# Kernel tuning notes

Hardware: AMD Instinct MI355X
Metric: run time of the kernel (lower is better)

The kernel has to match this reference:

```python
import jax, jax.numpy as jnp
import numpy as np

N, D, H, L, GHD, OUT = 512, 128, 4, 4, 32, 128  # nodes, input_dim, heads, layers, graph_hidden_dim, output_dim


def _xavier(key, shape):
    fan_in, fan_out = shape[0], shape[1]
    limit = float(np.sqrt(6.0 / (fan_in + fan_out)))
    return jax.random.uniform(key, shape, jnp.float32, -limit, limit)


def setup_inputs() -> dict:
    key = jax.random.key(0)
    ks = jax.random.split(key, 16)
    node_feat = jax.random.normal(ks[0], (N, D), jnp.float32)
    edge_feat = jax.random.normal(ks[1], (N, N, D), jnp.float32)
    adj = jax.random.uniform(ks[2], (H, N, N), jnp.float32)
    # per-(head,layer) edge weights: all [D, GHD]
    W_edge = _xavier(ks[3], (D, GHD))[None, None] * jnp.ones((H, L, 1, 1), jnp.float32)
    W_edge = jax.random.uniform(ks[3], (H, L, D, GHD), jnp.float32, -0.1, 0.1)
    # per-layer node weights (input dim grows by GHD each layer): [H, D + l*GHD, GHD]
    Wn0 = _xavier(ks[4], (D + 0 * GHD, GHD))[None] * jnp.ones((H, 1, 1), jnp.float32)
    Wn0 = jax.random.uniform(ks[4], (H, D + 0 * GHD, GHD), jnp.float32, -0.1, 0.1)
    Wn1 = jax.random.uniform(ks[5], (H, D + 1 * GHD, GHD), jnp.float32, -0.1, 0.1)
    Wn2 = jax.random.uniform(ks[6], (H, D + 2 * GHD, GHD), jnp.float32, -0.1, 0.1)
    Wn3 = jax.random.uniform(ks[7], (H, D + 3 * GHD, GHD), jnp.float32, -0.1, 0.1)
    # final linear: in = hidden_dim * head_num = L*GHD*H = 512, out = OUT
    W_lin = _xavier(ks[8], (L * GHD * H, OUT))
    b_lin = jnp.zeros((OUT,), jnp.float32)
    return {"node_feat": node_feat, "edge_feat": edge_feat, "adj": adj,
            "W_edge": W_edge, "Wn0": Wn0, "Wn1": Wn1, "Wn2": Wn2, "Wn3": Wn3,
            "W_lin": W_lin, "b_lin": b_lin}


def reference(node_feat, edge_feat, adj, W_edge, Wn0, Wn1, Wn2, Wn3, W_lin, b_lin):
    # mean over second node axis; einsum('ijk,kp->ijp') then mean(dim=1) == mean then matmul
    edge_mean = jnp.mean(edge_feat, axis=1)  # [N, D]
    Wn = [Wn0, Wn1, Wn2, Wn3]
    head_feats = []
    for h in range(H):
        A = adj[h]                         # [N, N]
        deg = jnp.sum(A, axis=1)           # [N]
        denom = (deg + (deg == 0).astype(deg.dtype))[:, None]  # zero-degree -> divide by 1
        outputs = node_feat
        cache = [node_feat]
        outs = []
        for l in range(L):
            e_out = edge_mean @ W_edge[h, l]            # [N, GHD]
            n_out = A @ (outputs @ Wn[l][h])            # chain_matmul(A, X, W)
            g = jax.nn.relu((e_out + n_out) / denom)    # [N, GHD]
            cache.append(g)
            outputs = jnp.concatenate(cache, axis=-1)
            outs.append(g)                              # dropout is eval-mode identity
        head_feats.append(jnp.concatenate(outs, axis=-1) + node_feat)  # [N, D]
    all_heads = jnp.concatenate(head_feats, axis=-1)    # [N, H*D]
    return all_heads @ W_lin + b_lin                    # [N, OUT]
```

## Files before the change

### kernel.cpp

```cpp
#include <hip/hip_runtime.h>
#include <cstddef>

#define NN 512
#define DD 128
#define HH 4
#define LL 4
#define GHD 32
#define OUTD 128

static constexpr size_t OFF_EP  = 0;
static constexpr size_t OFF_ANF = OFF_EP  + (size_t)4 * NN * DD;
static constexpr size_t OFF_DEN = OFF_ANF + (size_t)HH * NN * DD;
static constexpr size_t OFF_EO  = OFF_DEN + (size_t)HH * NN;
static constexpr size_t OFF_G   = OFF_EO  + (size_t)HH * LL * NN * GHD;
static constexpr size_t OFF_AG  = OFF_G   + (size_t)HH * LL * NN * GHD;

__global__ __launch_bounds__(256) void prep_kernel(
    const float* __restrict__ node_feat,
    const float* __restrict__ edge_feat,
    const float* __restrict__ adj,
    float* __restrict__ ws)
{
    const int t = threadIdx.x;
    const int b = blockIdx.x;
    __shared__ __align__(16) float smem[4 * NN + 256];

    if (b >= 512) {
        const int bb = b - 512;
        const int r  = bb >> 2;
        const int jq = bb & 3;
        const int q  = t & 31;
        const int g  = t >> 5;
        const float4* ef = reinterpret_cast<const float4*>(edge_feat)
                         + ((size_t)r * NN + (size_t)jq * 128) * (DD / 4);
        float4 acc; acc.x = acc.y = acc.z = acc.w = 0.f;
        #pragma unroll
        for (int k = 0; k < 16; ++k) {
            float4 v = ef[(size_t)(g + 8 * k) * (DD / 4) + q];
            acc.x += v.x; acc.y += v.y; acc.z += v.z; acc.w += v.w;
        }
        float4* red = reinterpret_cast<float4*>(smem);
        red[t] = acc;
        __syncthreads();
        for (int s = 128; s >= 32; s >>= 1) {
            if (t < s) {
                float4 o = red[t + s], m = red[t];
                m.x += o.x; m.y += o.y; m.z += o.z; m.w += o.w;
                red[t] = m;
            }
            __syncthreads();
        }
        if (t < 32)
            reinterpret_cast<float4*>(ws + OFF_EP + ((size_t)jq * NN + r) * DD)[t] = red[t];
    } else {
        const int h  = b >> 7;
        const int r0 = (b & 127) * 4;
        const float* A = adj + (size_t)h * NN * NN;
        float* Arow = smem;
        float* dred = smem + 4 * NN;

        for (int idx = t; idx < 4 * NN; idx += 256)
            Arow[idx] = A[(size_t)r0 * NN + idx];
        __syncthreads();

        {
            const int rr = t >> 6, lane = t & 63;
            float s = 0.f;
            #pragma unroll 8
            for (int j = lane; j < NN; j += 64) s += Arow[rr * NN + j];
            dred[t] = s;
            __syncthreads();
            if (t < 4) {
                float d = 0.f;
                for (int j = 0; j < 64; ++j) d += dred[t * 64 + j];
                ws[OFF_DEN + (size_t)h * NN + r0 + t] = d + (d == 0.f ? 1.f : 0.f);
            }
        }

        const int c  = t & 127;
        const int rb = t >> 7;
        float a0 = 0.f, a1 = 0.f;
        #pragma unroll 4
        for (int j = 0; j < NN; ++j) {
            float nf = node_feat[(size_t)j * DD + c];
            a0 += Arow[(rb + 0) * NN + j] * nf;
            a1 += Arow[(rb + 2) * NN + j] * nf;
        }
        float* anf = ws + OFF_ANF + ((size_t)h * NN + r0) * DD;
        anf[(rb + 0) * DD + c] = a0;
        anf[(rb + 2) * DD + c] = a1;
    }
}

__global__ __launch_bounds__(256) void eout_kernel(
    const float* __restrict__ W_edge,
    float* __restrict__ ws)
{
    const int b  = blockIdx.x;
    const int rg = b & 31;
    const int hl = b >> 5;
    const int r0 = rg * 16;
    const int t  = threadIdx.x;
    __shared__ float em[16 * DD];

    const float* P = ws + OFF_EP;
    for (int idx = t; idx < 16 * DD; idx += 256) {
        int r = r0 + (idx >> 7), k = idx & 127;
        size_t o = (size_t)r * DD + k;
        em[idx] = (P[o] + P[(size_t)NN * DD + o]
                 + P[2 * (size_t)NN * DD + o] + P[3 * (size_t)NN * DD + o])
                * (1.0f / (float)NN);
    }
    __syncthreads();

    const int c  = t & 31;
    const int rr = t >> 5;
    const float* We = W_edge + (size_t)hl * DD * GHD;
    float s0 = 0.f, s1 = 0.f;
    #pragma unroll 4
    for (int k = 0; k < DD; ++k) {
        float w = We[(size_t)k * GHD + c];
        s0 += em[rr * DD + k] * w;
        s1 += em[(rr + 8) * DD + k] * w;
    }
    float* eo = ws + OFF_EO + ((size_t)hl * NN + r0) * GHD;
    eo[(size_t)rr * GHD + c]       = s0;
    eo[(size_t)(rr + 8) * GHD + c] = s1;
}

template <int L>
__global__ __launch_bounds__(256) void layer_kernel(
    const float* __restrict__ adj,
    const float* __restrict__ Wn,
    float* __restrict__ ws)
{
    constexpr int KIN = DD + GHD * L;
    const int b   = blockIdx.x;
    const int h   = b >> 8;
    const int r0  = (b & 255) * 2;
    const int t   = threadIdx.x;
    const int rr  = t >> 7;
    const int sub = (t >> 5) & 3;
    const int c   = t & 31;
    const int r   = r0 + rr;

    const float* anf = ws + OFF_ANF;
    const float* den = ws + OFF_DEN;
    const float* eo  = ws + OFF_EO;
    float* G  = ws + OFF_G;
    float* AG = ws + OFF_AG;

    __shared__ float smem[256 + 64 + 256];
    float* agp = smem;
    float* agl = smem + 256;
    float* pp  = smem + 320;

    if (L > 0) {
        const float4* A4 = reinterpret_cast<const float4*>(
            adj + ((size_t)h * NN + r) * NN);
        const float* gp = G + (((size_t)h * LL + (L - 1)) * NN) * GHD;
        float s = 0.f;
        #pragma unroll 4
        for (int j4 = sub * 32; j4 < sub * 32 + 32; ++j4) {
            float4 a = A4[j4];
            const float* gj = gp + (size_t)j4 * 4 * GHD + c;
            s += a.x * gj[0] + a.y * gj[GHD] + a.z * gj[2 * GHD] + a.w * gj[3 * GHD];
        }
        agp[t] = s;
    }
    __syncthreads();
    if (L > 0 && sub == 0) {
        float ag = agp[rr * 128 + c] + agp[rr * 128 + 32 + c]
                 + agp[rr * 128 + 64 + c] + agp[rr * 128 + 96 + c];
        AG[(((size_t)h * 3 + (L - 1)) * NN + r) * GHD + c] = ag;
        agl[rr * GHD + c] = ag;
    }
    __syncthreads();

    float p = 0.f;
    {
        const float* Wnl = Wn + (size_t)h * KIN * GHD;
        const float* ar  = anf + ((size_t)h * NN + r) * DD;
        #pragma unroll 8
        for (int k = sub * 32; k < sub * 32 + 32; ++k)
            p += ar[k] * Wnl[(size_t)k * GHD + c];
        if (sub < L) {
            const float* agk = (sub == L - 1)
                ? (agl + rr * GHD)
                : (AG + (((size_t)h * 3 + sub) * NN + r) * GHD);
            const float* w = Wnl + (size_t)(DD + sub * GHD) * GHD + c;
            #pragma unroll 8
            for (int m = 0; m < GHD; ++m)
                p += agk[m] * w[(size_t)m * GHD];
        }
    }
    pp[t] = p;
    __syncthreads();
    if (sub == 0) {
        float tot = pp[rr * 128 + c] + pp[rr * 128 + 32 + c]
                  + pp[rr * 128 + 64 + c] + pp[rr * 128 + 96 + c]
                  + eo[(((size_t)h * LL + L) * NN + r) * GHD + c];
        float dn = den[(size_t)h * NN + r];
        float gv = tot / dn;
        gv = gv > 0.f ? gv : 0.f;
        G[(((size_t)h * LL + L) * NN + r) * GHD + c] = gv;
    }
}

__global__ __launch_bounds__(256) void final_kernel(
    const float* __restrict__ node_feat,
    const float* __restrict__ W_lin,
    const float* __restrict__ b_lin,
    const float* __restrict__ ws,
    float* __restrict__ out)
{
    const int b  = blockIdx.x;
    const int n  = b >> 1;
    const int oh = b & 1;
    const int t  = threadIdx.x;
    const int ol = t & 63;
    const int ks = t >> 6;
    const int o  = oh * 64 + ol;
    const float* G = ws + OFF_G;
    __shared__ float red[256];

    float p = 0.f;
    #pragma unroll
    for (int l = 0; l < LL; ++l) {
        const float* gr  = G + (((size_t)ks * LL + l) * NN + n) * GHD;
        const float* nfr = node_feat + (size_t)n * DD + l * GHD;
        const float* w   = W_lin + (size_t)(ks * DD + l * GHD) * OUTD + o;
        #pragma unroll 8
        for (int cc = 0; cc < GHD; ++cc)
            p += (gr[cc] + nfr[cc]) * w[(size_t)cc * OUTD];
    }
    red[t] = p;
    __syncthreads();
    if (ks == 0)
        out[(size_t)n * OUTD + o] =
            red[ol] + red[64 + ol] + red[128 + ol] + red[192 + ol] + b_lin[o];
}

extern "C" void kernel_launch(void* const* d_in, const int* in_sizes, int n_in,
                              void* d_out, int out_size, void* d_ws, size_t ws_size,
                              hipStream_t stream)
{
    const float* node_feat = (const float*)d_in[0];
    const float* edge_feat = (const float*)d_in[1];
    const float* adj       = (const float*)d_in[2];
    const float* W_edge    = (const float*)d_in[3];
    const float* Wn0       = (const float*)d_in[4];
    const float* Wn1       = (const float*)d_in[5];
    const float* Wn2       = (const float*)d_in[6];
    const float* Wn3       = (const float*)d_in[7];
    const float* W_lin     = (const float*)d_in[8];
    const float* b_lin     = (const float*)d_in[9];
    float* out = (float*)d_out;
    float* ws  = (float*)d_ws;

    hipLaunchKernelGGL(prep_kernel, dim3(512 + 2048), dim3(256), 0, stream,
                       node_feat, edge_feat, adj, ws);
    hipLaunchKernelGGL(eout_kernel, dim3(512), dim3(256), 0, stream, W_edge, ws);
    hipLaunchKernelGGL(layer_kernel<0>, dim3(1024), dim3(256), 0, stream, adj, Wn0, ws);
    hipLaunchKernelGGL(layer_kernel<1>, dim3(1024), dim3(256), 0, stream, adj, Wn1, ws);
    hipLaunchKernelGGL(layer_kernel<2>, dim3(1024), dim3(256), 0, stream, adj, Wn2, ws);
    hipLaunchKernelGGL(layer_kernel<3>, dim3(1024), dim3(256), 0, stream, adj, Wn3, ws);
    hipLaunchKernelGGL(final_kernel, dim3(1024), dim3(256), 0, stream,
                       node_feat, W_lin, b_lin, ws, out);
}
```

Baseline: 330.8 us.

## Fuse all stages into one cooperative persistent kernel with grid syncs

```diff
diff --git a/kernel.cpp b/kernel.cpp
--- a/kernel.cpp
+++ b/kernel.cpp
@@ -1,5 +1,8 @@
 #include <hip/hip_runtime.h>
+#include <hip/hip_cooperative_groups.h>
 #include <cstddef>
+
+namespace cg = cooperative_groups;
 
 #define NN 512
 #define DD 128
@@ -14,6 +17,249 @@
 static constexpr size_t OFF_EO  = OFF_DEN + (size_t)HH * NN;
 static constexpr size_t OFF_G   = OFF_EO  + (size_t)HH * LL * NN * GHD;
 static constexpr size_t OFF_AG  = OFF_G   + (size_t)HH * LL * NN * GHD;
+
+__device__ __forceinline__ void f4acc(float4& a, const float4& v) {
+    a.x += v.x; a.y += v.y; a.z += v.z; a.w += v.w;
+}
+
+__global__ __launch_bounds__(256, 2) void fused_kernel(
+    const float* __restrict__ node_feat,
+    const float* __restrict__ edge_feat,
+    const float* __restrict__ adj,
+    const float* __restrict__ W_edge,
+    const float* __restrict__ Wn0,
+    const float* __restrict__ Wn1,
+    const float* __restrict__ Wn2,
+    const float* __restrict__ Wn3,
+    const float* __restrict__ W_lin,
+    const float* __restrict__ b_lin,
+    float* __restrict__ ws,
+    float* __restrict__ out)
+{
+    cg::grid_group grid = cg::this_grid();
+    const int t = threadIdx.x;
+    const int b = blockIdx.x;
+
+    __shared__ __align__(16) float smem[8192];
+
+    float* EM  = ws + OFF_EP;
+    float* ANF = ws + OFF_ANF;
+    float* DEN = ws + OFF_DEN;
+    float* EO  = ws + OFF_EO;
+    float* G   = ws + OFF_G;
+    float* AG  = ws + OFF_AG;
+
+    {
+        const float4* efb = reinterpret_cast<const float4*>(edge_feat)
+                          + (size_t)b * (NN * DD / 4);
+        float4 a0{0,0,0,0}, a1{0,0,0,0}, a2{0,0,0,0}, a3{0,0,0,0};
+        #pragma unroll
+        for (int m = 0; m < 16; ++m) {
+            float4 v0 = efb[(4*m + 0) * 256 + t];
+            float4 v1 = efb[(4*m + 1) * 256 + t];
+            float4 v2 = efb[(4*m + 2) * 256 + t];
+            float4 v3 = efb[(4*m + 3) * 256 + t];
+            f4acc(a0, v0); f4acc(a1, v1); f4acc(a2, v2); f4acc(a3, v3);
+        }
+        f4acc(a0, a1); f4acc(a2, a3); f4acc(a0, a2);
+        float4* red = reinterpret_cast<float4*>(smem);
+        red[t] = a0;
+        __syncthreads();
+        if (t < 128) f4acc(red[t], red[t + 128]);
+        __syncthreads();
+        if (t < 64)  f4acc(red[t], red[t + 64]);
+        __syncthreads();
+        if (t < 32) {
+            float4 m = red[t];
+            f4acc(m, red[t + 32]);
+            const float inv = 1.0f / (float)NN;
+            m.x *= inv; m.y *= inv; m.z *= inv; m.w *= inv;
+            reinterpret_cast<float4*>(EM + (size_t)b * DD)[t] = m;
+        }
+        __syncthreads();
+    }
+
+    if (b < 128) {
+        const int h  = b >> 5;
+        const int r0 = (b & 31) * 16;
+        float4* As4 = reinterpret_cast<float4*>(smem);
+        const float4* Ad4 = reinterpret_cast<const float4*>(
+            adj + ((size_t)h * NN + r0) * NN);
+        #pragma unroll
+        for (int u = 0; u < 8; ++u) As4[t + u * 256] = Ad4[t + u * 256];
+        __syncthreads();
+        const float* Arow = smem;
+
+        {
+            const int rl = t >> 4, ln = t & 15;
+            float s = 0.f;
+            #pragma unroll 8
+            for (int j = ln; j < NN; j += 16) s += Arow[rl * NN + j];
+            #pragma unroll
+            for (int m = 8; m >= 1; m >>= 1) s += __shfl_xor(s, m);
+            if (ln == 0)
+                DEN[(size_t)h * NN + r0 + rl] = s + (s == 0.f ? 1.f : 0.f);
+        }
+
+        const int c = t & 127, rg = t >> 7;
+        float c0=0,c1=0,c2=0,c3=0,c4=0,c5=0,c6=0,c7=0;
+        #pragma unroll 4
+        for (int j = 0; j < NN; ++j) {
+            float nf = node_feat[(size_t)j * DD + c];
+            c0 += Arow[(rg +  0) * NN + j] * nf;
+            c1 += Arow[(rg +  2) * NN + j] * nf;
+            c2 += Arow[(rg +  4) * NN + j] * nf;
+            c3 += Arow[(rg +  6) * NN + j] * nf;
+            c4 += Arow[(rg +  8) * NN + j] * nf;
+            c5 += Arow[(rg + 10) * NN + j] * nf;
+            c6 += Arow[(rg + 12) * NN + j] * nf;
+            c7 += Arow[(rg + 14) * NN + j] * nf;
+        }
+        float* ab = ANF + ((size_t)h * NN + r0) * DD + c;
+        ab[(rg +  0) * DD] = c0; ab[(rg +  2) * DD] = c1;
+        ab[(rg +  4) * DD] = c2; ab[(rg +  6) * DD] = c3;
+        ab[(rg +  8) * DD] = c4; ab[(rg + 10) * DD] = c5;
+        ab[(rg + 12) * DD] = c6; ab[(rg + 14) * DD] = c7;
+    }
+
+    grid.sync();
+
+    const int h  = b >> 7;
+    const int r0 = (b & 127) * 4;
+    const int c  = t & 31;
+    const int ks = (t >> 5) & 1;
+    const int rr = t >> 6;
+    const int r  = r0 + rr;
+
+    float* emS   = smem;
+    float* anfS  = smem + 512;
+    float* aglS  = smem + 1024;
+    float* pred  = smem + 1152;
+    float* ArowS = smem + 1408;
+
+    emS[t]        = EM[((size_t)r0 + (t >> 7)) * DD + (t & 127)];
+    emS[t + 256]  = EM[((size_t)r0 + 2 + (t >> 7)) * DD + (t & 127)];
+    anfS[t]       = ANF[((size_t)h * NN + r0 + (t >> 7)) * DD + (t & 127)];
+    anfS[t + 256] = ANF[((size_t)h * NN + r0 + 2 + (t >> 7)) * DD + (t & 127)];
+    __syncthreads();
+
+    float eo0 = 0.f;
+    #pragma unroll
+    for (int l = 0; l < 4; ++l) {
+        const float* We = W_edge + ((size_t)(h * LL + l) * DD) * GHD;
+        float p = 0.f;
+        #pragma unroll 8
+        for (int k = ks * 64; k < ks * 64 + 64; ++k)
+            p += emS[rr * DD + k] * We[(size_t)k * GHD + c];
+        pred[t] = p;
+        __syncthreads();
+        if (ks == 0) {
+            float v = pred[t] + pred[t + 32];
+            if (l == 0) eo0 = v;
+            else EO[((size_t)(h * LL + l) * NN + r) * GHD + c] = v;
+        }
+        __syncthreads();
+    }
+    {
+        const float* W0 = Wn0 + (size_t)h * DD * GHD;
+        float p = 0.f;
+        #pragma unroll 8
+        for (int k = ks * 64; k < ks * 64 + 64; ++k)
+            p += anfS[rr * DD + k] * W0[(size_t)k * GHD + c];
+        pred[t] = p;
+        __syncthreads();
+        if (ks == 0) {
+            float v = pred[t] + pred[t + 32] + eo0;
+            v /= DEN[(size_t)h * NN + r];
+            v = v > 0.f ? v : 0.f;
+            G[((size_t)(h * LL + 0) * NN + r) * GHD + c] = v;
+        }
+    }
+
+    #pragma unroll
+    for (int l = 1; l < 4; ++l) {
+        grid.sync();
+        if (l == 1) {
+            float4* As4 = reinterpret_cast<float4*>(ArowS);
+            const float4* Ad4 = reinterpret_cast<const float4*>(
+                adj + ((size_t)h * NN + r0) * NN);
+            As4[t]       = Ad4[t];
+            As4[t + 256] = Ad4[t + 256];
+            __syncthreads();
+        }
+        {
+            const float* gp = G + ((size_t)(h * LL + l - 1) * NN) * GHD;
+            const float4* Ar4 = reinterpret_cast<const float4*>(ArowS);
+            float s = 0.f;
+            #pragma unroll 4
+            for (int j4 = ks * 64; j4 < ks * 64 + 64; ++j4) {
+                float4 a = Ar4[rr * 128 + j4];
+                const float* gj = gp + (size_t)j4 * 4 * GHD + c;
+                s += a.x * gj[0] + a.y * gj[GHD]
+                   + a.z * gj[2 * GHD] + a.w * gj[3 * GHD];
+            }
+            pred[t] = s;
+            __syncthreads();
+            if (ks == 0) {
+                float ag = pred[t] + pred[t + 32];
+                AG[((size_t)(h * 3 + l - 1) * NN + r) * GHD + c] = ag;
+                aglS[rr * GHD + c] = ag;
+            }
+            __syncthreads();
+        }
+        const float* Wnb = (l == 1) ? Wn1 : (l == 2) ? Wn2 : Wn3;
+        const float* Wnl = Wnb + (size_t)h * (DD + GHD * l) * GHD;
+        float p = 0.f;
+        #pragma unroll 8
+        for (int k = ks * 64; k < ks * 64 + 64; ++k)
+            p += anfS[rr * DD + k] * Wnl[(size_t)k * GHD + c];
+        #pragma unroll
+        for (int kk = 0; kk < l; ++kk) {
+            if ((kk & 1) == ks) {
+                const float* agv = (kk == l - 1)
+                    ? (aglS + rr * GHD)
+                    : (AG + ((size_t)(h * 3 + kk) * NN + r) * GHD);
+                const float* w = Wnl + ((size_t)(DD + kk * GHD)) * GHD + c;
+                #pragma unroll 8
+                for (int m = 0; m < GHD; ++m)
+                    p += agv[m] * w[(size_t)m * GHD];
+            }
+        }
+        pred[t] = p;
+        __syncthreads();
+        if (ks == 0) {
+            float v = pred[t] + pred[t + 32]
+                    + EO[((size_t)(h * LL + l) * NN + r) * GHD + c];
+            v /= DEN[(size_t)h * NN + r];
+            v = v > 0.f ? v : 0.f;
+            G[((size_t)(h * LL + l) * NN + r) * GHD + c] = v;
+        }
+    }
+
+    grid.sync();
+
+    {
+        const int n  = b;
+        const int o  = t & 127;
+        const int hs = t >> 7;
+        float p = 0.f;
+        for (int hh = hs; hh < HH; hh += 2) {
+            #pragma unroll
+            for (int l2 = 0; l2 < LL; ++l2) {
+                const float* gr  = G + ((size_t)(hh * LL + l2) * NN + n) * GHD;
+                const float* nfr = node_feat + (size_t)n * DD + l2 * GHD;
+                const float* w   = W_lin + (size_t)(hh * DD + l2 * GHD) * OUTD + o;
+                #pragma unroll 8
+                for (int cc = 0; cc < GHD; ++cc)
+                    p += (gr[cc] + nfr[cc]) * w[(size_t)cc * OUTD];
+            }
+        }
+        smem[t] = p;
+        __syncthreads();
+        if (hs == 0)
+            out[(size_t)n * OUTD + o] = smem[o] + smem[o + 128] + b_lin[o];
+    }
+}
 
 __global__ __launch_bounds__(256) void prep_kernel(
     const float* __restrict__ node_feat,
@@ -33,21 +279,17 @@
         const int g  = t >> 5;
         const float4* ef = reinterpret_cast<const float4*>(edge_feat)
                          + ((size_t)r * NN + (size_t)jq * 128) * (DD / 4);
-        float4 acc; acc.x = acc.y = acc.z = acc.w = 0.f;
+        float4 acc{0,0,0,0};
         #pragma unroll
         for (int k = 0; k < 16; ++k) {
             float4 v = ef[(size_t)(g + 8 * k) * (DD / 4) + q];
-            acc.x += v.x; acc.y += v.y; acc.z += v.z; acc.w += v.w;
+            f4acc(acc, v);
         }
         float4* red = reinterpret_cast<float4*>(smem);
         red[t] = acc;
         __syncthreads();
         for (int s = 128; s >= 32; s >>= 1) {
-            if (t < s) {
-                float4 o = red[t + s], m = red[t];
-                m.x += o.x; m.y += o.y; m.z += o.z; m.w += o.w;
-                red[t] = m;
-            }
+            if (t < s) f4acc(red[t], red[t + s]);
             __syncthreads();
         }
         if (t < 32)
@@ -62,7 +304,6 @@
         for (int idx = t; idx < 4 * NN; idx += 256)
             Arow[idx] = A[(size_t)r0 * NN + idx];
         __syncthreads();
-
         {
             const int rr = t >> 6, lane = t & 63;
             float s = 0.f;
@@ -76,7 +317,6 @@
                 ws[OFF_DEN + (size_t)h * NN + r0 + t] = d + (d == 0.f ? 1.f : 0.f);
             }
         }
-
         const int c  = t & 127;
         const int rb = t >> 7;
         float a0 = 0.f, a1 = 0.f;
@@ -258,13 +498,24 @@
     float* out = (float*)d_out;
     float* ws  = (float*)d_ws;
 
-    hipLaunchKernelGGL(prep_kernel, dim3(512 + 2048), dim3(256), 0, stream,
-                       node_feat, edge_feat, adj, ws);
-    hipLaunchKernelGGL(eout_kernel, dim3(512), dim3(256), 0, stream, W_edge, ws);
-    hipLaunchKernelGGL(layer_kernel<0>, dim3(1024), dim3(256), 0, stream, adj, Wn0, ws);
-    hipLaunchKernelGGL(layer_kernel<1>, dim3(1024), dim3(256), 0, stream, adj, Wn1, ws);
-    hipLaunchKernelGGL(layer_kernel<2>, dim3(1024), dim3(256), 0, stream, adj, Wn2, ws);
-    hipLaunchKernelGGL(layer_kernel<3>, dim3(1024), dim3(256), 0, stream, adj, Wn3, ws);
-    hipLaunchKernelGGL(final_kernel, dim3(1024), dim3(256), 0, stream,
-                       node_feat, W_lin, b_lin, ws, out);
-}
+    void* args[] = {
+        (void*)&node_feat, (void*)&edge_feat, (void*)&adj, (void*)&W_edge,
+        (void*)&Wn0, (void*)&Wn1, (void*)&Wn2, (void*)&Wn3,
+        (void*)&W_lin, (void*)&b_lin, (void*)&ws, (void*)&out
+    };
+    hipError_t rc = hipLaunchCooperativeKernel(
+        reinterpret_cast<void*>(fused_kernel),
+        dim3(512), dim3(256), args, 0, stream);
+
+    if (rc != hipSuccess) {
+        hipLaunchKernelGGL(prep_kernel, dim3(512 + 2048), dim3(256), 0, stream,
+                           node_feat, edge_feat, adj, ws);
+        hipLaunchKernelGGL(eout_kernel, dim3(512), dim3(256), 0, stream, W_edge, ws);
+        hipLaunchKernelGGL(layer_kernel<0>, dim3(1024), dim3(256), 0, stream, adj, Wn0, ws);
+        hipLaunchKernelGGL(layer_kernel<1>, dim3(1024), dim3(256), 0, stream, adj, Wn1, ws);
+        hipLaunchKernelGGL(layer_kernel<2>, dim3(1024), dim3(256), 0, stream, adj, Wn2, ws);
+        hipLaunchKernelGGL(layer_kernel<3>, dim3(1024), dim3(256), 0, stream, adj, Wn3, ws);
+        hipLaunchKernelGGL(final_kernel, dim3(1024), dim3(256), 0, stream,
+                           node_feat, W_lin, b_lin, ws, out);
+    }
+}
```

Measured after the change: 617.3 us. 1.87x slower.

## Fuse prep, edge-output and layer-0 into one kernel; fuse layer-3 with final linear

Applied to the files above, without the earlier changes.

```diff
diff --git a/kernel.cpp b/kernel.cpp
--- a/kernel.cpp
+++ b/kernel.cpp
@@ -8,124 +8,148 @@
 #define GHD 32
 #define OUTD 128
 
-static constexpr size_t OFF_EP  = 0;
-static constexpr size_t OFF_ANF = OFF_EP  + (size_t)4 * NN * DD;
+static constexpr size_t OFF_ANF = 0;
 static constexpr size_t OFF_DEN = OFF_ANF + (size_t)HH * NN * DD;
 static constexpr size_t OFF_EO  = OFF_DEN + (size_t)HH * NN;
 static constexpr size_t OFF_G   = OFF_EO  + (size_t)HH * LL * NN * GHD;
 static constexpr size_t OFF_AG  = OFF_G   + (size_t)HH * LL * NN * GHD;
 
-__global__ __launch_bounds__(256) void prep_kernel(
+__device__ __forceinline__ void f4acc(float4& a, const float4& v) {
+    a.x += v.x; a.y += v.y; a.z += v.z; a.w += v.w;
+}
+
+__global__ __launch_bounds__(256, 2) void k1_prep(
     const float* __restrict__ node_feat,
     const float* __restrict__ edge_feat,
     const float* __restrict__ adj,
+    const float* __restrict__ W_edge,
+    const float* __restrict__ Wn0,
     float* __restrict__ ws)
 {
+    const int r = blockIdx.x;
     const int t = threadIdx.x;
-    const int b = blockIdx.x;
-    __shared__ __align__(16) float smem[4 * NN + 256];
-
-    if (b >= 512) {
-        const int bb = b - 512;
-        const int r  = bb >> 2;
-        const int jq = bb & 3;
-        const int q  = t & 31;
-        const int g  = t >> 5;
-        const float4* ef = reinterpret_cast<const float4*>(edge_feat)
-                         + ((size_t)r * NN + (size_t)jq * 128) * (DD / 4);
-        float4 acc; acc.x = acc.y = acc.z = acc.w = 0.f;
-        #pragma unroll
-        for (int k = 0; k < 16; ++k) {
-            float4 v = ef[(size_t)(g + 8 * k) * (DD / 4) + q];
-            acc.x += v.x; acc.y += v.y; acc.z += v.z; acc.w += v.w;
-        }
-        float4* red = reinterpret_cast<float4*>(smem);
-        red[t] = acc;
-        __syncthreads();
-        for (int s = 128; s >= 32; s >>= 1) {
-            if (t < s) {
-                float4 o = red[t + s], m = red[t];
-                m.x += o.x; m.y += o.y; m.z += o.z; m.w += o.w;
-                red[t] = m;
+
+    __shared__ __align__(16) float4 red4[256];
+    __shared__ float ArowS[4 * NN];
+    __shared__ float emS[DD];
+    __shared__ float anfS[4 * DD];
+    __shared__ float eo0S[4 * GHD];
+    __shared__ float denS[4];
+    __shared__ float pred[256];
+
+    float* ANF = ws + OFF_ANF;
+    float* DEN = ws + OFF_DEN;
+    float* EO  = ws + OFF_EO;
+    float* G   = ws + OFF_G;
+
+    {
+        const float4* efb = reinterpret_cast<const float4*>(edge_feat)
+                          + (size_t)r * (NN * DD / 4);
+        const int m0 = r & 63;
+        float4 acc[8];
+        #pragma unroll
+        for (int u = 0; u < 8; ++u) acc[u] = float4{0, 0, 0, 0};
+        #pragma unroll
+        for (int batch = 0; batch < 4; ++batch) {
+            float4 v[16];
+            #pragma unroll
+            for (int u = 0; u < 16; ++u) {
+                int mm = (m0 + batch * 16 + u) & 63;
+                v[u] = efb[(size_t)mm * 256 + t];
             }
-            __syncthreads();
-        }
-        if (t < 32)
-            reinterpret_cast<float4*>(ws + OFF_EP + ((size_t)jq * NN + r) * DD)[t] = red[t];
-    } else {
-        const int h  = b >> 7;
-        const int r0 = (b & 127) * 4;
-        const float* A = adj + (size_t)h * NN * NN;
-        float* Arow = smem;
-        float* dred = smem + 4 * NN;
-
-        for (int idx = t; idx < 4 * NN; idx += 256)
-            Arow[idx] = A[(size_t)r0 * NN + idx];
-        __syncthreads();
-
-        {
-            const int rr = t >> 6, lane = t & 63;
-            float s = 0.f;
-            #pragma unroll 8
-            for (int j = lane; j < NN; j += 64) s += Arow[rr * NN + j];
-            dred[t] = s;
-            __syncthreads();
-            if (t < 4) {
-                float d = 0.f;
-                for (int j = 0; j < 64; ++j) d += dred[t * 64 + j];
-                ws[OFF_DEN + (size_t)h * NN + r0 + t] = d + (d == 0.f ? 1.f : 0.f);
-            }
-        }
-
-        const int c  = t & 127;
-        const int rb = t >> 7;
+            #pragma unroll
+            for (int u = 0; u < 16; ++u) f4acc(acc[u & 7], v[u]);
+        }
+        #pragma unroll
+        for (int u = 1; u < 8; ++u) f4acc(acc[0], acc[u]);
+        red4[t] = acc[0];
+        __syncthreads();
+        if (t < 128) f4acc(red4[t], red4[t + 128]);
+        __syncthreads();
+        if (t < 64)  f4acc(red4[t], red4[t + 64]);
+        __syncthreads();
+        if (t < 32) {
+            float4 m = red4[t];
+            f4acc(m, red4[t + 32]);
+            const float inv = 1.0f / (float)NN;
+            m.x *= inv; m.y *= inv; m.z *= inv; m.w *= inv;
+            reinterpret_cast<float4*>(emS)[t] = m;
+        }
+    }
+
+    {
+        float4* As4 = reinterpret_cast<float4*>(ArowS);
+        const float4* adj4 = reinterpret_cast<const float4*>(adj);
+        #pragma unroll
+        for (int u = 0; u < 2; ++u) {
+            int idx = u * 256 + t;
+            int h = idx >> 7, j4 = idx & 127;
+            As4[idx] = adj4[(size_t)h * (NN * NN / 4) + (size_t)r * (NN / 4) + j4];
+        }
+    }
+    __syncthreads();
+
+    {
+        const int w = t >> 6, ln = t & 63;
+        float s = 0.f;
+        #pragma unroll
+        for (int j = 0; j < 8; ++j) s += ArowS[w * NN + ln + j * 64];
+        #pragma unroll
+        for (int m = 32; m >= 1; m >>= 1) s += __shfl_xor(s, m);
+        if (ln == 0) {
+            float d = s + (s == 0.f ? 1.f : 0.f);
+            denS[w] = d;
+            DEN[(size_t)w * NN + r] = d;
+        }
+    }
+
+    {
+        const int c = t & 127, hp = t >> 7;
         float a0 = 0.f, a1 = 0.f;
-        #pragma unroll 4
+        #pragma unroll 8
         for (int j = 0; j < NN; ++j) {
             float nf = node_feat[(size_t)j * DD + c];
-            a0 += Arow[(rb + 0) * NN + j] * nf;
-            a1 += Arow[(rb + 2) * NN + j] * nf;
-        }
-        float* anf = ws + OFF_ANF + ((size_t)h * NN + r0) * DD;
-        anf[(rb + 0) * DD + c] = a0;
-        anf[(rb + 2) * DD + c] = a1;
-    }
-}
-
-__global__ __launch_bounds__(256) void eout_kernel(
-    const float* __restrict__ W_edge,
-    float* __restrict__ ws)
-{
-    const int b  = blockIdx.x;
-    const int rg = b & 31;
-    const int hl = b >> 5;
-    const int r0 = rg * 16;
-    const int t  = threadIdx.x;
-    __shared__ float em[16 * DD];
-
-    const float* P = ws + OFF_EP;
-    for (int idx = t; idx < 16 * DD; idx += 256) {
-        int r = r0 + (idx >> 7), k = idx & 127;
-        size_t o = (size_t)r * DD + k;
-        em[idx] = (P[o] + P[(size_t)NN * DD + o]
-                 + P[2 * (size_t)NN * DD + o] + P[3 * (size_t)NN * DD + o])
-                * (1.0f / (float)NN);
-    }
-    __syncthreads();
-
-    const int c  = t & 31;
-    const int rr = t >> 5;
-    const float* We = W_edge + (size_t)hl * DD * GHD;
-    float s0 = 0.f, s1 = 0.f;
-    #pragma unroll 4
-    for (int k = 0; k < DD; ++k) {
-        float w = We[(size_t)k * GHD + c];
-        s0 += em[rr * DD + k] * w;
-        s1 += em[(rr + 8) * DD + k] * w;
-    }
-    float* eo = ws + OFF_EO + ((size_t)hl * NN + r0) * GHD;
-    eo[(size_t)rr * GHD + c]       = s0;
-    eo[(size_t)(rr + 8) * GHD + c] = s1;
+            a0 += ArowS[hp * NN + j] * nf;
+            a1 += ArowS[(hp + 2) * NN + j] * nf;
+        }
+        anfS[hp * DD + c]       = a0;
+        anfS[(hp + 2) * DD + c] = a1;
+        ANF[((size_t)hp * NN + r) * DD + c]       = a0;
+        ANF[((size_t)(hp + 2) * NN + r) * DD + c] = a1;
+    }
+
+    {
+        const int c = t & 31, g = t >> 5;
+        float e0 = 0.f, e1 = 0.f;
+        #pragma unroll 8
+        for (int k = 0; k < DD; ++k) {
+            float e = emS[k];
+            e0 += e * W_edge[((size_t)g * DD + k) * GHD + c];
+            e1 += e * W_edge[((size_t)(g + 8) * DD + k) * GHD + c];
+        }
+        EO[((size_t)g * NN + r) * GHD + c]       = e0;
+        EO[((size_t)(g + 8) * NN + r) * GHD + c] = e1;
+        if ((g & 3) == 0)       eo0S[(g >> 2) * GHD + c]       = e0;
+        if (((g + 8) & 3) == 0) eo0S[((g + 8) >> 2) * GHD + c] = e1;
+    }
+    __syncthreads();
+
+    {
+        const int h = t >> 6, kh = (t >> 5) & 1, c = t & 31;
+        const float* W0 = Wn0 + (size_t)h * DD * GHD;
+        float p = 0.f;
+        #pragma unroll 8
+        for (int k = kh * 64; k < kh * 64 + 64; ++k)
+            p += anfS[h * DD + k] * W0[(size_t)k * GHD + c];
+        pred[t] = p;
+        __syncthreads();
+        if (kh == 0) {
+            float v = p + pred[t + 32] + eo0S[h * GHD + c];
+            v /= denS[h];
+            v = v > 0.f ? v : 0.f;
+            G[((size_t)(h * LL + 0) * NN + r) * GHD + c] = v;
+        }
+    }
 }
 
 template <int L>
@@ -155,12 +179,12 @@
     float* agl = smem + 256;
     float* pp  = smem + 320;
 
-    if (L > 0) {
+    {
         const float4* A4 = reinterpret_cast<const float4*>(
             adj + ((size_t)h * NN + r) * NN);
         const float* gp = G + (((size_t)h * LL + (L - 1)) * NN) * GHD;
         float s = 0.f;
-        #pragma unroll 4
+        #pragma unroll 8
         for (int j4 = sub * 32; j4 < sub * 32 + 32; ++j4) {
             float4 a = A4[j4];
             const float* gj = gp + (size_t)j4 * 4 * GHD + c;
@@ -169,7 +193,7 @@
         agp[t] = s;
     }
     __syncthreads();
-    if (L > 0 && sub == 0) {
+    if (sub == 0) {
         float ag = agp[rr * 128 + c] + agp[rr * 128 + 32 + c]
                  + agp[rr * 128 + 64 + c] + agp[rr * 128 + 96 + c];
         AG[(((size_t)h * 3 + (L - 1)) * NN + r) * GHD + c] = ag;
@@ -185,13 +209,13 @@
         for (int k = sub * 32; k < sub * 32 + 32; ++k)
             p += ar[k] * Wnl[(size_t)k * GHD + c];
         if (sub < L) {
-            const float* agk = (sub == L - 1)
+            const float* agv = (sub == L - 1)
                 ? (agl + rr * GHD)
                 : (AG + (((size_t)h * 3 + sub) * NN + r) * GHD);
             const float* w = Wnl + (size_t)(DD + sub * GHD) * GHD + c;
             #pragma unroll 8
             for (int m = 0; m < GHD; ++m)
-                p += agk[m] * w[(size_t)m * GHD];
+                p += agv[m] * w[(size_t)m * GHD];
         }
     }
     pp[t] = p;
@@ -207,38 +231,131 @@
     }
 }
 
-__global__ __launch_bounds__(256) void final_kernel(
+__global__ __launch_bounds__(256) void k4_last(
     const float* __restrict__ node_feat,
+    const float* __restrict__ adj,
+    const float* __restrict__ Wn3,
     const float* __restrict__ W_lin,
     const float* __restrict__ b_lin,
     const float* __restrict__ ws,
     float* __restrict__ out)
 {
-    const int b  = blockIdx.x;
-    const int n  = b >> 1;
-    const int oh = b & 1;
-    const int t  = threadIdx.x;
-    const int ol = t & 63;
-    const int ks = t >> 6;
-    const int o  = oh * 64 + ol;
-    const float* G = ws + OFF_G;
-    __shared__ float red[256];
-
-    float p = 0.f;
-    #pragma unroll
-    for (int l = 0; l < LL; ++l) {
-        const float* gr  = G + (((size_t)ks * LL + l) * NN + n) * GHD;
-        const float* nfr = node_feat + (size_t)n * DD + l * GHD;
-        const float* w   = W_lin + (size_t)(ks * DD + l * GHD) * OUTD + o;
-        #pragma unroll 8
-        for (int cc = 0; cc < GHD; ++cc)
-            p += (gr[cc] + nfr[cc]) * w[(size_t)cc * OUTD];
-    }
-    red[t] = p;
-    __syncthreads();
-    if (ks == 0)
-        out[(size_t)n * OUTD + o] =
-            red[ol] + red[64 + ol] + red[128 + ol] + red[192 + ol] + b_lin[o];
+    const int r = blockIdx.x;
+    const int t = threadIdx.x;
+
+    __shared__ float ArowS[4 * NN];
+    __shared__ float anfS[4 * DD];
+    __shared__ float nfS[DD];
+    __shared__ float ag2S[4 * GHD];
+    __shared__ float g3S[4 * GHD];
+    __shared__ float denS[4];
+    __shared__ float Xs[4 * DD];
+    __shared__ float pred[256];
+
+    const float* ANF = ws + OFF_ANF;
+    const float* DEN = ws + OFF_DEN;
+    const float* EO  = ws + OFF_EO;
+    const float* G   = ws + OFF_G;
+    const float* AG  = ws + OFF_AG;
+
+    {
+        float4* As4 = reinterpret_cast<float4*>(ArowS);
+        const float4* adj4 = reinterpret_cast<const float4*>(adj);
+        #pragma unroll
+        for (int u = 0; u < 2; ++u) {
+            int idx = u * 256 + t;
+            int h = idx >> 7, j4 = idx & 127;
+            As4[idx] = adj4[(size_t)h * (NN * NN / 4) + (size_t)r * (NN / 4) + j4];
+        }
+        #pragma unroll
+        for (int u = 0; u < 2; ++u) {
+            int idx = u * 256 + t;
+            int h = idx >> 7, k = idx & 127;
+            anfS[idx] = ANF[((size_t)h * NN + r) * DD + k];
+        }
+        if (t < DD) nfS[t] = node_feat[(size_t)r * DD + t];
+        if (t < 4)  denS[t] = DEN[(size_t)t * NN + r];
+    }
+    __syncthreads();
+
+    {
+        const int h = t >> 6, jh = (t >> 5) & 1, c = t & 31;
+        const float* g2 = G + ((size_t)(h * LL + 2) * NN) * GHD;
+        float s = 0.f;
+        #pragma unroll 8
+        for (int j = jh * 256; j < jh * 256 + 256; ++j)
+            s += ArowS[h * NN + j] * g2[(size_t)j * GHD + c];
+        pred[t] = s;
+        __syncthreads();
+        if (jh == 0) ag2S[h * GHD + c] = s + pred[t + 32];
+        __syncthreads();
+    }
+
+    {
+        const int h = t >> 6, kh = (t >> 5) & 1, c = t & 31;
+        const float* W3 = Wn3 + (size_t)h * 224 * GHD;
+        float p = 0.f;
+        #pragma unroll 8
+        for (int k = kh * 64; k < kh * 64 + 64; ++k)
+            p += anfS[h * DD + k] * W3[(size_t)k * GHD + c];
+        if (kh == 0) {
+            const float* ag0 = AG + ((size_t)(h * 3 + 0) * NN + r) * GHD;
+            const float* w   = W3 + (size_t)DD * GHD + c;
+            #pragma unroll 8
+            for (int m = 0; m < GHD; ++m)
+                p += ag0[m] * w[(size_t)m * GHD];
+            const float* w2 = W3 + (size_t)(DD + 2 * GHD) * GHD + c;
+            #pragma unroll 8
+            for (int m = 0; m < GHD; ++m)
+                p += ag2S[h * GHD + m] * w2[(size_t)m * GHD];
+        } else {
+            const float* ag1 = AG + ((size_t)(h * 3 + 1) * NN + r) * GHD;
+            const float* w   = W3 + (size_t)(DD + GHD) * GHD + c;
+            #pragma unroll 8
+            for (int m = 0; m < GHD; ++m)
+                p += ag1[m] * w[(size_t)m * GHD];
+        }
+        pred[t] = p;
+        __syncthreads();
+        if (kh == 0) {
+            float v = p + pred[t + 32]
+                    + EO[((size_t)(h * LL + 3) * NN + r) * GHD + c];
+            v /= denS[h];
+            v = v > 0.f ? v : 0.f;
+            g3S[h * GHD + c] = v;
+        }
+        __syncthreads();
+    }
+
+    {
+        #pragma unroll
+        for (int u = 0; u < 2; ++u) {
+            int idx = u * 256 + t;
+            int h = idx >> 7, k = idx & 127;
+            int l = k >> 5, cc = k & 31;
+            float gv = (l < 3)
+                ? G[((size_t)(h * LL + l) * NN + r) * GHD + cc]
+                : g3S[h * GHD + cc];
+            Xs[idx] = gv + nfS[k];
+        }
+    }
+    __syncthreads();
+
+    {
+        const int o = t & 127, hs = t >> 7;
+        float p = 0.f;
+        #pragma unroll
+        for (int hh = hs; hh < HH; hh += 2) {
+            const float* w = W_lin + (size_t)hh * DD * OUTD + o;
+            #pragma unroll 8
+            for (int k = 0; k < DD; ++k)
+                p += Xs[hh * DD + k] * w[(size_t)k * OUTD];
+        }
+        pred[t] = p;
+        __syncthreads();
+        if (hs == 0)
+            out[(size_t)r * OUTD + o] = p + pred[t + 128] + b_lin[o];
+    }
 }
 
 extern "C" void kernel_launch(void* const* d_in, const int* in_sizes, int n_in,
@@ -258,13 +375,10 @@
     float* out = (float*)d_out;
     float* ws  = (float*)d_ws;
 
-    hipLaunchKernelGGL(prep_kernel, dim3(512 + 2048), dim3(256), 0, stream,
-                       node_feat, edge_feat, adj, ws);
-    hipLaunchKernelGGL(eout_kernel, dim3(512), dim3(256), 0, stream, W_edge, ws);
-    hipLaunchKernelGGL(layer_kernel<0>, dim3(1024), dim3(256), 0, stream, adj, Wn0, ws);
+    hipLaunchKernelGGL(k1_prep, dim3(NN), dim3(256), 0, stream,
+                       node_feat, edge_feat, adj, W_edge, Wn0, ws);
     hipLaunchKernelGGL(layer_kernel<1>, dim3(1024), dim3(256), 0, stream, adj, Wn1, ws);
     hipLaunchKernelGGL(layer_kernel<2>, dim3(1024), dim3(256), 0, stream, adj, Wn2, ws);
-    hipLaunchKernelGGL(layer_kernel<3>, dim3(1024), dim3(256), 0, stream, adj, Wn3, ws);
-    hipLaunchKernelGGL(final_kernel, dim3(1024), dim3(256), 0, stream,
-                       node_feat, W_lin, b_lin, ws, out);
-}
+    hipLaunchKernelGGL(k4_last, dim3(NN), dim3(256), 0, stream,
+                       node_feat, adj, Wn3, W_lin, b_lin, ws, out);
+}
```

Result: faster. 314.4 us (-5.0%).
